# Kernel optimization log

Hardware: AMD Instinct MI355X
Metric: run time of the kernel (lower is better)

The kernel has to match this reference:

```python
import jax, jax.numpy as jnp
import numpy as np

N, C_IN, C_OUT, K = 8192, 128, 128, 3


def setup_inputs() -> dict:
    key = jax.random.key(0)
    k1, k2, k3 = jax.random.split(key, 3)
    x = jax.random.normal(k1, (N, C_IN), dtype=jnp.float32)
    # scale L by 1/sqrt(N) so the Chebyshev recurrence stays numerically tame
    L = jax.random.normal(k2, (N, N), dtype=jnp.float32) / np.sqrt(N).astype(np.float32)
    # stacked per-order linear weights, W[j] has shape [out, in] like nn.Linear.weight
    W = jax.random.normal(k3, (K, C_OUT, C_IN), dtype=jnp.float32) / np.sqrt(C_IN).astype(np.float32)
    return {"x": x, "L": L, "W": W}


def reference(x, L, W):
    # Chebyshev polynomial recurrence: T_0 = x, T_1 = L x, T_j = 2 L T_{j-1} - T_{j-2}
    # out = sum_j T_j @ W[j].T
    k = W.shape[0]  # static
    T0 = x
    T1 = L @ x
    out = T0 @ W[0].T
    if k > 1:
        out = out + T1 @ W[1].T
    for j in range(2, k):
        T2 = 2.0 * (L @ T1) - T0
        out = out + T2 @ W[j].T
        T0, T1 = T1, T2
    return out
```

## Files before the change

### kernel.cpp

```cpp
#include <hip/hip_runtime.h>

typedef __attribute__((ext_vector_type(8))) short short8;
typedef __attribute__((ext_vector_type(4))) float float4_t;
typedef __attribute__((ext_vector_type(4))) unsigned short ushort4_t;

#define NR 8192
#define C 128
#define SPLITK 4
#define KCHUNK (NR / SPLITK)
#define BK 64
#define STEPS (KCHUNK / BK)

__device__ unsigned short g_xbT[(size_t)C * NR];
__device__ unsigned short g_T1b[(size_t)NR * C];
__device__ unsigned short g_T1bT[(size_t)C * NR];
__device__ unsigned short g_Wb[3 * C * C];
__device__ float g_part[(size_t)SPLITK * NR * C];

__device__ __forceinline__ unsigned short f2bf(float f) {
  union { float f; unsigned u; } v; v.f = f;
  unsigned r = v.u + 0x7fffu + ((v.u >> 16) & 1u);
  return (unsigned short)(r >> 16);
}
__device__ __forceinline__ unsigned pk2(float a, float b) {
  union { float f; unsigned u; } x, y; x.f = a; y.f = b;
  unsigned ra = x.u + 0x7fffu + ((x.u >> 16) & 1u);
  unsigned rb = y.u + 0x7fffu + ((y.u >> 16) & 1u);
  return (ra >> 16) | (rb & 0xffff0000u);
}
__device__ __forceinline__ short8 cvt8(float4_t f0, float4_t f1) {
  union { unsigned u[4]; short8 s; } r;
  r.u[0] = pk2(f0[0], f0[1]); r.u[1] = pk2(f0[2], f0[3]);
  r.u[2] = pk2(f1[0], f1[1]); r.u[3] = pk2(f1[2], f1[3]);
  return r.s;
}

typedef __attribute__((address_space(3))) unsigned lds_uint;
typedef const __attribute__((address_space(1))) unsigned glob_uint;
__device__ __forceinline__ void gload_lds16(const void* g, void* l) {
  __builtin_amdgcn_global_load_lds((glob_uint*)g, (lds_uint*)l, 16, 0, 0);
}

__global__ void cvt_w(const float* __restrict__ W) {
  int i = (blockIdx.x * 256 + threadIdx.x) * 4;
  float4_t v = *(const float4_t*)(W + i);
  ushort4_t h; h[0]=f2bf(v[0]); h[1]=f2bf(v[1]); h[2]=f2bf(v[2]); h[3]=f2bf(v[3]);
  *(ushort4_t*)(g_Wb + i) = h;
}

__global__ void transpose_x(const float* __restrict__ x) {
  __shared__ unsigned short xt[64][72];
  int r0 = blockIdx.x * 64;
  int c0 = blockIdx.y * 64;
  int t = threadIdx.x;
  int rr = t >> 4;
  int cc = (t & 15) * 4;
#pragma unroll
  for (int i = 0; i < 4; i++) {
    int row = i * 16 + rr;
    float4_t v = *(const float4_t*)(x + (size_t)(r0 + row) * C + c0 + cc);
    ushort4_t h; h[0]=f2bf(v[0]); h[1]=f2bf(v[1]); h[2]=f2bf(v[2]); h[3]=f2bf(v[3]);
    *(ushort4_t*)(&xt[row][cc]) = h;
  }
  __syncthreads();
  int c = t >> 2, q = t & 3;
  unsigned short* dst = g_xbT + (size_t)(c0 + c) * NR + r0 + q * 16;
#pragma unroll
  for (int seg = 0; seg < 2; seg++) {
    short8 h;
#pragma unroll
    for (int j = 0; j < 8; j++) h[j] = (short)xt[q * 16 + seg * 8 + j][c];
    *(short8*)(dst + seg * 8) = h;
  }
}

__global__ __launch_bounds__(256, 2) void gemm_cheb(const float* __restrict__ L, int which) {
  const unsigned short* __restrict__ BT = which ? g_T1bT : g_xbT;
  __shared__ __attribute__((aligned(16))) float          As[2][64 * BK];
  __shared__ __attribute__((aligned(16))) unsigned short Bs[2][128 * BK];
  int tid = threadIdx.x;
  int wave = tid >> 6, lane = tid & 63;
  int l15 = lane & 15, lq = lane >> 4;
  int m0 = blockIdx.x * 64;
  int kb = blockIdx.y * KCHUNK;

  const float* pA[4];
#pragma unroll
  for (int i = 0; i < 4; i++) {
    int U = (wave * 4 + i) * 64 + lane;
    int row = U >> 4, p = U & 15;
    pA[i] = L + (size_t)(m0 + row) * NR + kb + ((p ^ (row & 15)) << 2);
  }
  const unsigned short* pB[4];
#pragma unroll
  for (int i = 0; i < 4; i++) {
    int U = (wave * 4 + i) * 64 + lane;
    int n = U >> 3, p = U & 7;
    pB[i] = BT + (size_t)n * NR + kb + ((p ^ (n & 7)) << 3);
  }

  float4_t acc[8];
#pragma unroll
  for (int ni = 0; ni < 8; ni++) acc[ni] = (float4_t){0.f, 0.f, 0.f, 0.f};

  #define ISSUE(buf)                                                         \
    do {                                                                     \
      _Pragma("unroll")                                                      \
      for (int i = 0; i < 4; i++)                                            \
        gload_lds16(pA[i], (char*)&As[buf][0] + (wave * 4 + i) * 1024);      \
      _Pragma("unroll")                                                      \
      for (int i = 0; i < 4; i++)                                            \
        gload_lds16(pB[i], (char*)&Bs[buf][0] + (wave * 4 + i) * 1024);      \
      _Pragma("unroll")                                                      \
      for (int i = 0; i < 4; i++) { pA[i] += BK; pB[i] += BK; }              \
    } while (0)

  #define COMPUTE(buf)                                                       \
    do {                                                                     \
      _Pragma("unroll")                                                      \
      for (int ki = 0; ki < 2; ki++) {                                       \
        int row = wave * 16 + l15;                                           \
        int u0 = (ki << 3) | (lq << 1);                                      \
        int p0 = u0 ^ (row & 15);                                            \
        float4_t f0 = *(const float4_t*)((const char*)&As[buf][0] + row * 256 + p0 * 16);        \
        float4_t f1 = *(const float4_t*)((const char*)&As[buf][0] + row * 256 + (p0 ^ 1) * 16);  \
        short8 a = cvt8(f0, f1);                                             \
        _Pragma("unroll")                                                    \
        for (int ni = 0; ni < 8; ni++) {                                     \
          int n = ni * 16 + l15;                                             \
          int pb = ((ki << 2) | lq) ^ (n & 7);                               \
          short8 b = *(const short8*)((const char*)&Bs[buf][0] + n * 128 + pb * 16);             \
          acc[ni] = __builtin_amdgcn_mfma_f32_16x16x32_bf16(a, b, acc[ni], 0, 0, 0);             \
        }                                                                    \
      }                                                                      \
    } while (0)

  ISSUE(0);
  for (int step = 0; step < STEPS - 1; step++) {
    int p = step & 1;
    ISSUE(p ^ 1);
    asm volatile("s_waitcnt vmcnt(8)" ::: "memory");
    asm volatile("s_barrier" ::: "memory");
    COMPUTE(p);
    asm volatile("s_barrier" ::: "memory");
  }
  asm volatile("s_waitcnt vmcnt(0)" ::: "memory");
  asm volatile("s_barrier" ::: "memory");
  COMPUTE((STEPS - 1) & 1);

  float* po = g_part + (size_t)blockIdx.y * NR * C;
#pragma unroll
  for (int ni = 0; ni < 8; ni++)
#pragma unroll
    for (int r = 0; r < 4; r++)
      po[(size_t)(m0 + wave * 16 + lq * 4 + r) * C + ni * 16 + l15] = acc[ni][r];
  #undef ISSUE
  #undef COMPUTE
}

__global__ void reduce_t1() {
  __shared__ unsigned short tile[16][136];
  int r0 = blockIdx.x * 16;
  int t = threadIdx.x;
#pragma unroll
  for (int e = 0; e < 2; e++) {
    int linear = e * 1024 + t * 4;
    int r = linear >> 7, c = linear & 127;
    float4_t s = (float4_t){0.f, 0.f, 0.f, 0.f};
#pragma unroll
    for (int p = 0; p < SPLITK; p++)
      s += *(const float4_t*)(g_part + (size_t)p * NR * C + (size_t)(r0 + r) * C + c);
    ushort4_t h; h[0]=f2bf(s[0]); h[1]=f2bf(s[1]); h[2]=f2bf(s[2]); h[3]=f2bf(s[3]);
    *(ushort4_t*)(g_T1b + (size_t)(r0 + r) * C + c) = h;
    *(ushort4_t*)(&tile[r][c]) = h;
  }
  __syncthreads();
  int c = t >> 1, half = t & 1;
  short8 h;
#pragma unroll
  for (int j = 0; j < 8; j++) h[j] = (short)tile[half * 8 + j][c];
  *(short8*)(g_T1bT + (size_t)c * NR + r0 + half * 8) = h;
}

__global__ __launch_bounds__(256) void epilogue(const float* __restrict__ x,
                                                float* __restrict__ out) {
  __shared__ unsigned short t2[32][136];
  int r0 = blockIdx.x * 32;
  int t = threadIdx.x;
#pragma unroll
  for (int e = 0; e < 4; e++) {
    int linear = e * 1024 + t * 4;
    int r = linear >> 7, c = linear & 127;
    float4_t s = (float4_t){0.f, 0.f, 0.f, 0.f};
#pragma unroll
    for (int p = 0; p < SPLITK; p++)
      s += *(const float4_t*)(g_part + (size_t)p * NR * C + (size_t)(r0 + r) * C + c);
    float4_t xv = *(const float4_t*)(x + (size_t)(r0 + r) * C + c);
    float4_t t2v = 2.0f * s - xv;
    ushort4_t h; h[0]=f2bf(t2v[0]); h[1]=f2bf(t2v[1]); h[2]=f2bf(t2v[2]); h[3]=f2bf(t2v[3]);
    *(ushort4_t*)(&t2[r][c]) = h;
  }
  __syncthreads();

  int wave = t >> 6, lane = t & 63, l15 = lane & 15, lq = lane >> 4;
  int mf = wave & 1, nh = wave >> 1;
  int m0r = r0 + mf * 16;
  float4_t acc[4];
#pragma unroll
  for (int ni = 0; ni < 4; ni++) acc[ni] = (float4_t){0.f, 0.f, 0.f, 0.f};

#pragma unroll
  for (int ks = 0; ks < 4; ks++) {
    int k0 = ks * 32 + lq * 8;
    const float* px = x + (size_t)(m0r + l15) * C + k0;
    float4_t f0 = *(const float4_t*)px;
    float4_t f1 = *(const float4_t*)(px + 4);
    short8 a0 = cvt8(f0, f1);
    short8 a1 = *(const short8*)(g_T1b + (size_t)(m0r + l15) * C + k0);
    short8 a2 = *(const short8*)(&t2[mf * 16 + l15][k0]);
#pragma unroll
    for (int ni = 0; ni < 4; ni++) {
      int n = nh * 64 + ni * 16 + l15;
      const unsigned short* pw = g_Wb + (size_t)n * C + k0;
      short8 w0 = *(const short8*)(pw);
      short8 w1 = *(const short8*)(pw + C * C);
      short8 w2 = *(const short8*)(pw + 2 * C * C);
      acc[ni] = __builtin_amdgcn_mfma_f32_16x16x32_bf16(a0, w0, acc[ni], 0, 0, 0);
      acc[ni] = __builtin_amdgcn_mfma_f32_16x16x32_bf16(a1, w1, acc[ni], 0, 0, 0);
      acc[ni] = __builtin_amdgcn_mfma_f32_16x16x32_bf16(a2, w2, acc[ni], 0, 0, 0);
    }
  }
#pragma unroll
  for (int ni = 0; ni < 4; ni++)
#pragma unroll
    for (int r = 0; r < 4; r++)
      out[(size_t)(m0r + lq * 4 + r) * C + nh * 64 + ni * 16 + l15] = acc[ni][r];
}

extern "C" void kernel_launch(void* const* d_in, const int* in_sizes, int n_in,
                              void* d_out, int out_size, void* d_ws, size_t ws_size,
                              hipStream_t stream) {
  const float* x = (const float*)d_in[0];
  const float* L = (const float*)d_in[1];
  const float* W = (const float*)d_in[2];
  float* out = (float*)d_out;

  cvt_w<<<48, 256, 0, stream>>>(W);
  transpose_x<<<dim3(128, 2), 256, 0, stream>>>(x);
  gemm_cheb<<<dim3(128, SPLITK), 256, 0, stream>>>(L, 0);
  reduce_t1<<<512, 256, 0, stream>>>();
  gemm_cheb<<<dim3(128, SPLITK), 256, 0, stream>>>(L, 1);
  epilogue<<<256, 256, 0, stream>>>(x, out);
}
```

Baseline: 508.0 us.

## Cache bf16 copy of L in first GEMM and reuse it in second GEMM

The first L·x GEMM now writes its bf16-converted L tiles to a global buffer. A new second GEMM reads L directly as bf16, halving its A-operand traffic and skipping the conversion. Split-K is raised from 4 to 8 to expose more parallelism, and gemm2 targets higher occupancy. The cost is an extra 128 MB write in the first pass, a larger partial-sum buffer and a larger reduction.

```diff
diff --git a/kernel.cpp b/kernel.cpp
--- a/kernel.cpp
+++ b/kernel.cpp
@@ -6,7 +6,7 @@
 
 #define NR 8192
 #define C 128
-#define SPLITK 4
+#define SPLITK 8
 #define KCHUNK (NR / SPLITK)
 #define BK 64
 #define STEPS (KCHUNK / BK)
@@ -15,6 +15,7 @@
 __device__ unsigned short g_T1b[(size_t)NR * C];
 __device__ unsigned short g_T1bT[(size_t)C * NR];
 __device__ unsigned short g_Wb[3 * C * C];
+__device__ unsigned short g_Lb[(size_t)NR * NR];
 __device__ float g_part[(size_t)SPLITK * NR * C];
 
 __device__ __forceinline__ unsigned short f2bf(float f) {
@@ -74,8 +75,7 @@
   }
 }
 
-__global__ __launch_bounds__(256, 2) void gemm_cheb(const float* __restrict__ L, int which) {
-  const unsigned short* __restrict__ BT = which ? g_T1bT : g_xbT;
+__global__ __launch_bounds__(256, 2) void gemm1(const float* __restrict__ L) {
   __shared__ __attribute__((aligned(16))) float          As[2][64 * BK];
   __shared__ __attribute__((aligned(16))) unsigned short Bs[2][128 * BK];
   int tid = threadIdx.x;
@@ -96,14 +96,15 @@
   for (int i = 0; i < 4; i++) {
     int U = (wave * 4 + i) * 64 + lane;
     int n = U >> 3, p = U & 7;
-    pB[i] = BT + (size_t)n * NR + kb + ((p ^ (n & 7)) << 3);
-  }
+    pB[i] = g_xbT + (size_t)n * NR + kb + ((p ^ (n & 7)) << 3);
+  }
+  unsigned short* pw = g_Lb + (size_t)(m0 + wave * 16 + l15) * NR + kb + lq * 8;
 
   float4_t acc[8];
 #pragma unroll
   for (int ni = 0; ni < 8; ni++) acc[ni] = (float4_t){0.f, 0.f, 0.f, 0.f};
 
-  #define ISSUE(buf)                                                         \
+  #define ISSUE1(buf)                                                        \
     do {                                                                     \
       _Pragma("unroll")                                                      \
       for (int i = 0; i < 4; i++)                                            \
@@ -115,7 +116,7 @@
       for (int i = 0; i < 4; i++) { pA[i] += BK; pB[i] += BK; }              \
     } while (0)
 
-  #define COMPUTE(buf)                                                       \
+  #define COMPUTE1(buf)                                                      \
     do {                                                                     \
       _Pragma("unroll")                                                      \
       for (int ki = 0; ki < 2; ki++) {                                       \
@@ -125,6 +126,95 @@
         float4_t f0 = *(const float4_t*)((const char*)&As[buf][0] + row * 256 + p0 * 16);        \
         float4_t f1 = *(const float4_t*)((const char*)&As[buf][0] + row * 256 + (p0 ^ 1) * 16);  \
         short8 a = cvt8(f0, f1);                                             \
+        *(short8*)(pw + ki * 32) = a;       \
+        _Pragma("unroll")                                                    \
+        for (int ni = 0; ni < 8; ni++) {                                     \
+          int n = ni * 16 + l15;                                             \
+          int pb = ((ki << 2) | lq) ^ (n & 7);                               \
+          short8 b = *(const short8*)((const char*)&Bs[buf][0] + n * 128 + pb * 16);             \
+          acc[ni] = __builtin_amdgcn_mfma_f32_16x16x32_bf16(a, b, acc[ni], 0, 0, 0);             \
+        }                                                                    \
+      }                                                                      \
+      pw += BK;                                                              \
+    } while (0)
+
+  ISSUE1(0);
+  ISSUE1(1);
+  asm volatile("s_waitcnt vmcnt(8)" ::: "memory");
+  asm volatile("s_barrier" ::: "memory");
+  COMPUTE1(0);
+  asm volatile("s_barrier" ::: "memory");
+  for (int step = 1; step < STEPS - 1; step++) {
+    int p = step & 1;
+    ISSUE1(p ^ 1);
+    asm volatile("s_waitcnt vmcnt(10)" ::: "memory");
+    asm volatile("s_barrier" ::: "memory");
+    COMPUTE1(p);
+    asm volatile("s_barrier" ::: "memory");
+  }
+  asm volatile("s_waitcnt vmcnt(2)" ::: "memory");
+  asm volatile("s_barrier" ::: "memory");
+  COMPUTE1((STEPS - 1) & 1);
+
+  float* po = g_part + (size_t)blockIdx.y * NR * C;
+#pragma unroll
+  for (int ni = 0; ni < 8; ni++)
+#pragma unroll
+    for (int r = 0; r < 4; r++)
+      po[(size_t)(m0 + wave * 16 + lq * 4 + r) * C + ni * 16 + l15] = acc[ni][r];
+  #undef ISSUE1
+  #undef COMPUTE1
+}
+
+__global__ __launch_bounds__(256, 3) void gemm2() {
+  __shared__ __attribute__((aligned(16))) unsigned short As[2][64 * BK];
+  __shared__ __attribute__((aligned(16))) unsigned short Bs[2][128 * BK];
+  int tid = threadIdx.x;
+  int wave = tid >> 6, lane = tid & 63;
+  int l15 = lane & 15, lq = lane >> 4;
+  int m0 = blockIdx.x * 64;
+  int kb = blockIdx.y * KCHUNK;
+
+  const unsigned short* pA[2];
+#pragma unroll
+  for (int i = 0; i < 2; i++) {
+    int U = (wave * 2 + i) * 64 + lane;
+    int row = U >> 3, p = U & 7;
+    pA[i] = g_Lb + (size_t)(m0 + row) * NR + kb + ((p ^ (row & 7)) << 3);
+  }
+  const unsigned short* pB[4];
+#pragma unroll
+  for (int i = 0; i < 4; i++) {
+    int U = (wave * 4 + i) * 64 + lane;
+    int n = U >> 3, p = U & 7;
+    pB[i] = g_T1bT + (size_t)n * NR + kb + ((p ^ (n & 7)) << 3);
+  }
+
+  float4_t acc[8];
+#pragma unroll
+  for (int ni = 0; ni < 8; ni++) acc[ni] = (float4_t){0.f, 0.f, 0.f, 0.f};
+
+  #define ISSUE2(buf)                                                        \
+    do {                                                                     \
+      _Pragma("unroll")                                                      \
+      for (int i = 0; i < 2; i++)                                            \
+        gload_lds16(pA[i], (char*)&As[buf][0] + (wave * 2 + i) * 1024);      \
+      _Pragma("unroll")                                                      \
+      for (int i = 0; i < 4; i++)                                            \
+        gload_lds16(pB[i], (char*)&Bs[buf][0] + (wave * 4 + i) * 1024);      \
+      _Pragma("unroll")                                                      \
+      for (int i = 0; i < 2; i++) pA[i] += BK;                               \
+      _Pragma("unroll")                                                      \
+      for (int i = 0; i < 4; i++) pB[i] += BK;                               \
+    } while (0)
+
+  #define COMPUTE2(buf)                                                      \
+    do {                                                                     \
+      _Pragma("unroll")                                                      \
+      for (int ki = 0; ki < 2; ki++) {                                       \
+        int row = wave * 16 + l15;                                           \
+        int pa = ((ki << 2) | lq) ^ (row & 7);                               \
+        short8 a = *(const short8*)((const char*)&As[buf][0] + row * 128 + pa * 16);             \
         _Pragma("unroll")                                                    \
         for (int ni = 0; ni < 8; ni++) {                                     \
           int n = ni * 16 + l15;                                             \
@@ -135,18 +225,23 @@
       }                                                                      \
     } while (0)
 
-  ISSUE(0);
-  for (int step = 0; step < STEPS - 1; step++) {
+  ISSUE2(0);
+  ISSUE2(1);
+  asm volatile("s_waitcnt vmcnt(6)" ::: "memory");
+  asm volatile("s_barrier" ::: "memory");
+  COMPUTE2(0);
+  asm volatile("s_barrier" ::: "memory");
+  for (int step = 1; step < STEPS - 1; step++) {
     int p = step & 1;
-    ISSUE(p ^ 1);
-    asm volatile("s_waitcnt vmcnt(8)" ::: "memory");
+    ISSUE2(p ^ 1);
+    asm volatile("s_waitcnt vmcnt(6)" ::: "memory");
     asm volatile("s_barrier" ::: "memory");
-    COMPUTE(p);
+    COMPUTE2(p);
     asm volatile("s_barrier" ::: "memory");
   }
   asm volatile("s_waitcnt vmcnt(0)" ::: "memory");
   asm volatile("s_barrier" ::: "memory");
-  COMPUTE((STEPS - 1) & 1);
+  COMPUTE2((STEPS - 1) & 1);
 
   float* po = g_part + (size_t)blockIdx.y * NR * C;
 #pragma unroll
@@ -154,8 +249,8 @@
 #pragma unroll
     for (int r = 0; r < 4; r++)
       po[(size_t)(m0 + wave * 16 + lq * 4 + r) * C + ni * 16 + l15] = acc[ni][r];
-  #undef ISSUE
-  #undef COMPUTE
+  #undef ISSUE2
+  #undef COMPUTE2
 }
 
 __global__ void reduce_t1() {
@@ -247,8 +342,8 @@
 
   cvt_w<<<48, 256, 0, stream>>>(W);
   transpose_x<<<dim3(128, 2), 256, 0, stream>>>(x);
-  gemm_cheb<<<dim3(128, SPLITK), 256, 0, stream>>>(L, 0);
+  gemm1<<<dim3(128, SPLITK), 256, 0, stream>>>(L);
   reduce_t1<<<512, 256, 0, stream>>>();
-  gemm_cheb<<<dim3(128, SPLITK), 256, 0, stream>>>(L, 1);
+  gemm2<<<dim3(128, SPLITK), 256, 0, stream>>>();
   epilogue<<<256, 256, 0, stream>>>(x, out);
 }
```

Result: slower. 561.4 us (+10.5%).
